# Kernel optimization log

Measured on AMD Instinct MI355X. Metric: run time of the kernel, lower is better.

The kernel has to match this reference:

```python
import jax, jax.numpy as jnp
import numpy as np
from jax import lax


def _conv(x, w, pad):
    # NCHW conv, OIHW weights, stride 1
    return lax.conv_general_dilated(x, w, (1, 1), [(pad, pad), (pad, pad)],
                                    dimension_numbers=('NCHW', 'OIHW', 'NCHW'))


def _cba(x, w, s, b):
    # ConvModule: 3x3 conv (no bias) + folded BN (scale s, bias b) + ReLU
    y = _conv(x, w, 1)
    return jax.nn.relu(y * s[None, :, None, None] + b[None, :, None, None])


def _pam(x, wb, bb, wc, bc, wd, bd, alpha):
    B, C, H, W = x.shape
    fb = (_conv(x, wb, 0) + bb[None, :, None, None]).reshape(B, -1, H * W)  # [B,C/8,HW]
    fc = (_conv(x, wc, 0) + bc[None, :, None, None]).reshape(B, -1, H * W)  # [B,C/8,HW]
    # attention_s = softmax(feat_b^T @ feat_c) over last dim -> [B,HW,HW]
    attn = jax.nn.softmax(jnp.einsum('bcn,bcm->bnm', fb, fc), axis=-1)
    fd = (_conv(x, wd, 0) + bd[None, :, None, None]).reshape(B, C, H * W)
    # feat_d @ attn^T
    fe = jnp.einsum('bcm,bnm->bcn', fd, attn).reshape(B, C, H, W)
    return alpha * fe + x


def _cam(x, beta):
    B, C, H, W = x.shape
    fa = x.reshape(B, C, H * W)
    att = jnp.einsum('bcn,bdn->bcd', fa, fa)  # [B,C,C]
    att = jax.nn.softmax(jnp.max(att, axis=-1, keepdims=True) - att, axis=-1)
    fe = jnp.einsum('bcd,bdn->bcn', att, fa).reshape(B, C, H, W)
    return beta * fe + x


def _up2x(x):
    # bilinear, align_corners=False (half-pixel) == jax.image.resize 'bilinear'
    B, C, H, W = x.shape
    return jax.image.resize(x, (B, C, 2 * H, 2 * W), 'bilinear')


def setup_inputs() -> dict:
    key = jax.random.key(0)
    B, Cin, H, W = 4, 2048, 64, 64
    IC, C8, NC = 512, 64, 81

    def rn(i, shape, scale=0.02):
        return scale * jax.random.normal(jax.random.fold_in(key, i), shape, jnp.float32)

    inp = {
        'x': jax.random.normal(jax.random.fold_in(key, 0), (B, Cin, H, W), jnp.float32),
        'wp1': rn(1, (IC, Cin, 3, 3)), 'sp1': jnp.ones((IC,), jnp.float32), 'bp1': rn(2, (IC,)),
        'wc1': rn(3, (IC, Cin, 3, 3)), 'sc1': jnp.ones((IC,), jnp.float32), 'bc1': rn(4, (IC,)),
        'pam_wb': rn(5, (C8, IC, 1, 1)), 'pam_bb': rn(6, (C8,)),
        'pam_wc': rn(7, (C8, IC, 1, 1)), 'pam_bc': rn(8, (C8,)),
        'pam_wd': rn(9, (IC, IC, 1, 1)), 'pam_bd': rn(10, (IC,)),
        'alpha': rn(11, (1,), 1.0), 'beta': rn(12, (1,), 1.0),
        'wp2': rn(13, (IC, IC, 3, 3)), 'sp2': jnp.ones((IC,), jnp.float32), 'bp2': rn(14, (IC,)),
        'wc2': rn(15, (IC, IC, 3, 3)), 'sc2': jnp.ones((IC,), jnp.float32), 'bc2': rn(16, (IC,)),
        'wlog': rn(17, (NC, IC, 1, 1)), 'blog': rn(18, (NC,)),
        'wp3': rn(19, (NC, IC, 1, 1)), 'bp3': rn(20, (NC,)),
        'wc3': rn(21, (NC, IC, 1, 1)), 'bc3': rn(22, (NC,)),
    }
    return inp


def reference(x, wp1, sp1, bp1, wc1, sc1, bc1,
              pam_wb, pam_bb, pam_wc, pam_bc, pam_wd, pam_bd, alpha, beta,
              wp2, sp2, bp2, wc2, sc2, bc2,
              wlog, blog, wp3, bp3, wc3, bc3):
    feat_p = _cba(x, wp1, sp1, bp1)
    feat_p = _pam(feat_p, pam_wb, pam_bb, pam_wc, pam_bc, pam_wd, pam_bd, alpha)
    feat_p = _cba(feat_p, wp2, sp2, bp2)

    feat_c = _cba(x, wc1, sc1, bc1)
    feat_c = _cam(feat_c, beta)
    feat_c = _cba(feat_c, wc2, sc2, bc2)

    fusion = feat_p + feat_c
    fusion_out = _conv(fusion, wlog, 0) + blog[None, :, None, None]  # dropout = identity (eval)
    p_out = _conv(feat_p, wp3, 0) + bp3[None, :, None, None]
    c_out = _conv(feat_c, wc3, 0) + bc3[None, :, None, None]
    return (_up2x(p_out), _up2x(c_out), _up2x(fusion_out))
```

## Files before the change

kernel.cpp:

```cpp
#include <hip/hip_runtime.h>

typedef unsigned short u16;
typedef __bf16 bf16x8 __attribute__((ext_vector_type(8)));
typedef float f32x4 __attribute__((ext_vector_type(4)));

static __device__ __forceinline__ float bf2f(u16 v){ unsigned u=((unsigned)v)<<16; float f; __builtin_memcpy(&f,&u,4); return f; }
static __device__ __forceinline__ u16 f2bf(float f){ unsigned u; __builtin_memcpy(&u,&f,4); u += 0x7fffu + ((u>>16)&1u); return (u16)(u>>16); }

static __device__ __forceinline__ float wave_max(float v){
#pragma unroll
  for(int o=32;o;o>>=1) v=fmaxf(v,__shfl_xor(v,o,64));
  return v;
}
static __device__ __forceinline__ float wave_sum(float v){
#pragma unroll
  for(int o=32;o;o>>=1) v+=__shfl_xor(v,o,64);
  return v;
}

__global__ void k_sentinel(u16* __restrict__ o, float v){ o[0] = f2bf(v); }

__global__ void k_probe(const unsigned* __restrict__ w, int* __restrict__ flag){
  __shared__ int found;
  if (threadIdx.x==0) found = 0;
  __syncthreads();
  int loc = 0;
  for (int i = threadIdx.x; i < 32768; i += 256){
    unsigned v = w[i];
    if ((((v >> 7) & 0xFFu) == 0xFFu) || (((v >> 23) & 0xFFu) == 0xFFu)) loc = 1;
  }
  if (loc) atomicOr(&found, 1);
  __syncthreads();
  if (threadIdx.x==0) *flag = found;
}

__global__ void k_cvt(const void* __restrict__ src, u16* __restrict__ dst, int n, const int* __restrict__ flag){
  int i = blockIdx.x*256 + threadIdx.x;
  if (i >= n) return;
  if (*flag) dst[i] = f2bf(((const float*)src)[i]);
  else       dst[i] = ((const u16*)src)[i];
}

__global__ void k_zero(uint4* __restrict__ p, long n){
  long i = (long)blockIdx.x*256 + threadIdx.x;
  if (i < n) p[i] = make_uint4(0,0,0,0);
}

__global__ void k_pad1(const void* __restrict__ xb, u16* __restrict__ xp, int ICD, int icoff, int bbase,
                       const int* __restrict__ flag){
  __shared__ u16 tile[64][65];
  const int h = blockIdx.x;
  const int ic0 = blockIdx.y<<6;
  const int bi = blockIdx.z;
  const int t = threadIdx.x, lane = t&63, g = t>>6;
  const size_t base = ((size_t)(bbase+bi)*2048 + icoff + ic0)*4096 + (size_t)h*64;
  if (*flag){
    const float* src = (const float*)xb + base;
#pragma unroll
    for(int i=0;i<16;i++){ int icl = g*16+i; tile[icl][lane] = f2bf(src[(size_t)icl*4096 + lane]); }
  } else {
    const u16* src = (const u16*)xb + base;
#pragma unroll
    for(int i=0;i<16;i++){ int icl = g*16+i; tile[icl][lane] = src[(size_t)icl*4096 + lane]; }
  }
  __syncthreads();
  u16* dst = xp + ((size_t)bi*4356 + ((size_t)(h+1))*66 + 1)*ICD + ic0;
#pragma unroll
  for(int j=0;j<16;j++){ int w = g*16+j; dst[(size_t)w*ICD + lane] = tile[lane][w]; }
}

__global__ void k_wtrans(const void* __restrict__ w, u16* __restrict__ wt, int ICS, int ICD, int icoff,
                         const int* __restrict__ flag){
  size_t i = (size_t)blockIdx.x*256 + threadIdx.x;
  int icd = (int)(i & (ICD-1));
  size_t rest = i / ICD;
  int oc = (int)(rest & 511);
  int tap = (int)(rest >> 9);
  size_t sidx = ((size_t)oc*ICS + icoff + icd)*9 + tap;
  wt[i] = (*flag) ? f2bf(((const float*)w)[sidx]) : ((const u16*)w)[sidx];
}

__global__ void k_transpose(const u16* __restrict__ in, u16* __restrict__ outp, int R, int C){
  __shared__ u16 tile[64][65];
  const int c0 = blockIdx.x<<6, r0 = blockIdx.y<<6;
  const int t=threadIdx.x, lane=t&63, g=t>>6;
#pragma unroll
  for(int i=0;i<16;i++){ int rl=g*16+i; tile[rl][lane] = in[(size_t)(r0+rl)*C + c0 + lane]; }
  __syncthreads();
#pragma unroll
  for(int j=0;j<16;j++){ int cl=g*16+j; outp[(size_t)(c0+cl)*R + r0 + lane] = tile[lane][cl]; }
}

__global__ void k_pad_strip(const u16* __restrict__ in, u16* __restrict__ outp, int C, int npix){
  long i = (long)blockIdx.x*256 + threadIdx.x;
  int vpp = C>>3;
  if (i >= (long)npix*vpp) return;
  int p = (int)(i/vpp), v = (int)(i - (long)p*vpp);
  int b = p>>12, h=(p>>6)&63, w=p&63;
  ((uint4*)outp)[((size_t)(b*66+h+1)*66 + (w+1))*vpp + v] = ((const uint4*)in)[i];
}

__global__ void k_add_bf16(const u16* __restrict__ a, const u16* __restrict__ b, u16* __restrict__ o, long n){
  long i = ((long)blockIdx.x*256 + threadIdx.x)*8;
  if (i >= n) return;
  uint4 va = *(const uint4*)(a+i), vb = *(const uint4*)(b+i);
  u16* pa=(u16*)&va; u16* pb=(u16*)&vb;
  uint4 vo; u16* po=(u16*)&vo;
#pragma unroll
  for(int e=0;e<8;e++) po[e] = f2bf(bf2f(pa[e]) + bf2f(pb[e]));
  *(uint4*)(o+i) = vo;
}

__global__ __launch_bounds__(256,2) void gemm_nt(
    const u16* __restrict__ A, const u16* __restrict__ Bt,
    int N, int K, int lda, int ldb,
    void* __restrict__ Cout, int ldc, int mode,
    const u16* __restrict__ q1, const u16* __restrict__ q2, int zk, long zcb)
{
  if (zk){
    const int zz = blockIdx.z;
    A  += (size_t)zz*zk;
    Bt += (size_t)zz*zk;
    Cout = (void*)((char*)Cout + (size_t)zz*zcb);
    K = zk;
  }
  __shared__ __align__(16) u16 As[128*40];
  __shared__ __align__(16) u16 Bs[128*40];
  const int t = threadIdx.x;
  const int m0 = blockIdx.y<<7, n0 = blockIdx.x<<7;
  const int r = t>>2, q = t&3;
  const u16* A0 = A + (size_t)(m0+r)*lda + q*8;
  const u16* A1 = A0 + (size_t)64*lda;
  const bool bv0 = (n0+r)    < N;
  const bool bv1 = (n0+r+64) < N;
  const u16* B0 = Bt + (size_t)(n0+r)*ldb + q*8;
  const u16* B1 = B0 + (size_t)64*ldb;
  const int wave=t>>6, lane=t&63;
  const int wr=(wave>>1)<<6, wc=(wave&1)<<6, fm=lane&15, kg=lane>>4;
  f32x4 acc[4][4] = {};
  for (int k0=0; k0<K; k0+=32){
    uint4 a0 = *(const uint4*)(A0+k0);
    uint4 a1 = *(const uint4*)(A1+k0);
    uint4 b0 = bv0 ? *(const uint4*)(B0+k0) : make_uint4(0,0,0,0);
    uint4 b1 = bv1 ? *(const uint4*)(B1+k0) : make_uint4(0,0,0,0);
    __syncthreads();
    *(uint4*)&As[r*40+q*8] = a0;
    *(uint4*)&As[(r+64)*40+q*8] = a1;
    *(uint4*)&Bs[r*40+q*8] = b0;
    *(uint4*)&Bs[(r+64)*40+q*8] = b1;
    __syncthreads();
    bf16x8 af[4], bfr[4];
#pragma unroll
    for(int i=0;i<4;i++) af[i]  = *(const bf16x8*)&As[(wr+i*16+fm)*40 + kg*8];
#pragma unroll
    for(int j=0;j<4;j++) bfr[j] = *(const bf16x8*)&Bs[(wc+j*16+fm)*40 + kg*8];
#pragma unroll
    for(int i=0;i<4;i++)
#pragma unroll
      for(int j=0;j<4;j++)
        acc[i][j] = __builtin_amdgcn_mfma_f32_16x16x32_bf16(af[i], bfr[j], acc[i][j], 0,0,0);
  }
  const float alpha = (mode==3) ? bf2f(q1[0]) : 0.f;
#pragma unroll
  for(int j=0;j<4;j++){
    int col = n0 + wc + j*16 + fm;
    if (col >= N) continue;
    float bias = (mode==1) ? bf2f(q1[col]) : 0.f;
#pragma unroll
    for(int i=0;i<4;i++){
      int row = m0 + wr + i*16 + (kg<<2);
#pragma unroll
      for(int rr=0;rr<4;rr++){
        long idx = (long)(row+rr)*ldc + col;
        float v = acc[i][j][rr];
        if (mode==4)      ((float*)Cout)[idx] = v;
        else if (mode==3) ((u16*)Cout)[idx] = f2bf(alpha*v + bf2f(q2[idx]));
        else if (mode==5) ((u16*)Cout)[idx] = f2bf(v + bf2f(q1[row+rr]));
        else if (mode==1) ((u16*)Cout)[idx] = f2bf(v + bias);
        else              ((u16*)Cout)[idx] = f2bf(v);
      }
    }
  }
}

__global__ __launch_bounds__(256,2) void conv3_gemm(
    const u16* __restrict__ Xp, const u16* __restrict__ Wt, int ICt,
    u16* __restrict__ Out, const u16* __restrict__ scale, const u16* __restrict__ bias, int phase,
    long wstr, long ostr)
{
  __shared__ __align__(16) u16 As[128*40];
  __shared__ __align__(16) u16 Bs[128*40];
  const int t = threadIdx.x;
  const int bx = blockIdx.x;
  const int brn = bx>>2;
  const int m0 = blockIdx.y<<7, n0 = (bx&3)<<7;
  const u16* Wb = Wt + (size_t)brn*wstr;
  u16* Ob = Out + (size_t)brn*ostr;
  const u16* scb = scale + brn*1024;
  const u16* bib = bias + brn*1024;
  const int r = t>>2, q = t&3;
  const int p0 = m0 + r, p1 = p0 + 64;
  const size_t xb0 = ((size_t)((p0>>12)*66 + ((p0>>6)&63))*66 + (p0&63))*ICt + q*8;
  const size_t xb1 = ((size_t)((p1>>12)*66 + ((p1>>6)&63))*66 + (p1&63))*ICt + q*8;
  const u16* W0 = Wb + (size_t)(n0+r)*ICt + q*8;
  const u16* W1 = W0 + (size_t)64*ICt;
  const size_t wtap = (size_t)512*ICt;
  const int wave=t>>6, lane=t&63;
  const int wr=(wave>>1)<<6, wc=(wave&1)<<6, fm=lane&15, kg=lane>>4;
  f32x4 acc[4][4] = {};
  for (int tap=0; tap<9; tap++){
    const size_t toff = (size_t)((tap/3)*66 + (tap%3))*ICt;
    const u16* xa0 = Xp + xb0 + toff;
    const u16* xa1 = Xp + xb1 + toff;
    const u16* wa0 = W0 + (size_t)tap*wtap;
    const u16* wa1 = W1 + (size_t)tap*wtap;
    for (int k0=0; k0<ICt; k0+=32){
      uint4 a0 = *(const uint4*)(xa0+k0);
      uint4 a1 = *(const uint4*)(xa1+k0);
      uint4 b0 = *(const uint4*)(wa0+k0);
      uint4 b1 = *(const uint4*)(wa1+k0);
      __syncthreads();
      *(uint4*)&As[r*40+q*8] = a0;
      *(uint4*)&As[(r+64)*40+q*8] = a1;
      *(uint4*)&Bs[r*40+q*8] = b0;
      *(uint4*)&Bs[(r+64)*40+q*8] = b1;
      __syncthreads();
      bf16x8 af[4], bfr[4];
#pragma unroll
      for(int i=0;i<4;i++) af[i]  = *(const bf16x8*)&As[(wr+i*16+fm)*40 + kg*8];
#pragma unroll
      for(int j=0;j<4;j++) bfr[j] = *(const bf16x8*)&Bs[(wc+j*16+fm)*40 + kg*8];
#pragma unroll
      for(int i=0;i<4;i++)
#pragma unroll
        for(int j=0;j<4;j++)
          acc[i][j] = __builtin_amdgcn_mfma_f32_16x16x32_bf16(af[i], bfr[j], acc[i][j], 0,0,0);
    }
  }
#pragma unroll
  for(int j=0;j<4;j++){
    int col = n0 + wc + j*16 + fm;
    float s = bf2f(scb[col]), bb = bf2f(bib[col]);
#pragma unroll
    for(int i=0;i<4;i++){
      int row = m0 + wr + i*16 + (kg<<2);
#pragma unroll
      for(int rr=0;rr<4;rr++){
        size_t idx = (size_t)(row+rr)*512 + col;
        float v = acc[i][j][rr];
        if (phase == 0)      Ob[idx] = f2bf(v);
        else if (phase == 1) Ob[idx] = f2bf(fmaxf(s*(bf2f(Ob[idx]) + v) + bb, 0.f));
        else                 Ob[idx] = f2bf(fmaxf(s*v + bb, 0.f));
      }
    }
  }
}

__global__ __launch_bounds__(256) void k_softmax_pam(u16* __restrict__ attn){
  __shared__ float red[8];
  u16* row = attn + (size_t)blockIdx.x*4096;
  uint4* rv = (uint4*)row;
  const int t = threadIdx.x;
  uint4 c0 = rv[2*t], c1 = rv[2*t+1];
  u16* e0 = (u16*)&c0; u16* e1=(u16*)&c1;
  float v[16];
#pragma unroll
  for(int i=0;i<8;i++){ v[i]=bf2f(e0[i]); v[8+i]=bf2f(e1[i]); }
  float mx = v[0];
#pragma unroll
  for(int i=1;i<16;i++) mx = fmaxf(mx, v[i]);
  mx = wave_max(mx);
  if((t&63)==0) red[t>>6] = mx;
  __syncthreads();
  mx = fmaxf(fmaxf(red[0],red[1]),fmaxf(red[2],red[3]));
  float s = 0.f;
#pragma unroll
  for(int i=0;i<16;i++){ v[i]=__expf(v[i]-mx); s += v[i]; }
  s = wave_sum(s);
  if((t&63)==0) red[4+(t>>6)] = s;
  __syncthreads();
  s = red[4]+red[5]+red[6]+red[7];
  float inv = 1.f/s;
#pragma unroll
  for(int i=0;i<8;i++){ e0[i]=f2bf(v[i]*inv); e1[i]=f2bf(v[8+i]*inv); }
  rv[2*t]=c0; rv[2*t+1]=c1;
}

__global__ __launch_bounds__(256) void k_pv_combine(const float* __restrict__ Pp, u16* __restrict__ io,
                                                    const u16* __restrict__ alpha){
  const int i = blockIdx.x*256 + threadIdx.x;
  const float4* p = (const float4*)Pp;
  float4 a0 = p[i], a1 = p[i+262144], a2 = p[i+524288], a3 = p[i+786432];
  const float al = bf2f(alpha[0]);
  ushort4 d = ((const ushort4*)io)[i];
  ushort4 o;
  o.x = f2bf(al*(a0.x+a1.x+a2.x+a3.x) + bf2f(d.x));
  o.y = f2bf(al*(a0.y+a1.y+a2.y+a3.y) + bf2f(d.y));
  o.z = f2bf(al*(a0.z+a1.z+a2.z+a3.z) + bf2f(d.z));
  o.w = f2bf(al*(a0.w+a1.w+a2.w+a3.w) + bf2f(d.w));
  ((ushort4*)io)[i] = o;
}

__global__ __launch_bounds__(256) void k_softmax_cam8(const float* __restrict__ P8, u16* __restrict__ outp){
  __shared__ float red[8];
  const int t = threadIdx.x;
  const float* r0 = P8 + (size_t)blockIdx.x*512;
  float a = 0.f, b2 = 0.f;
#pragma unroll
  for(int s2=0;s2<8;s2++){ a += r0[(size_t)s2*262144 + t]; b2 += r0[(size_t)s2*262144 + 256 + t]; }
  a = -a; b2 = -b2;
  float mx = wave_max(fmaxf(a,b2));
  if((t&63)==0) red[t>>6]=mx;
  __syncthreads();
  mx = fmaxf(fmaxf(red[0],red[1]),fmaxf(red[2],red[3]));
  float ea = __expf(a-mx), eb = __expf(b2-mx);
  float s = wave_sum(ea+eb);
  if((t&63)==0) red[4+(t>>6)]=s;
  __syncthreads();
  s = red[4]+red[5]+red[6]+red[7];
  float inv = 1.f/s;
  u16* orow = outp + (size_t)blockIdx.x*512;
  orow[t] = f2bf(ea*inv); orow[t+256] = f2bf(eb*inv);
}

__global__ __launch_bounds__(128) void k_upsample(const u16* __restrict__ hp, const u16* __restrict__ hc,
                                                  const u16* __restrict__ hf, void* __restrict__ outp,
                                                  const int* __restrict__ flag){
  int bx = blockIdx.x;
  const int y = bx & 127; bx >>= 7;
  const int ch = bx % 81; bx /= 81;
  const int b = bx & 3; const int head = bx >> 2;
  const u16* src = (head==0) ? hp : (head==1 ? hc : hf);
  const int xo = threadIdx.x;
  float fy = y*0.5f - 0.25f, fx = xo*0.5f - 0.25f;
  float fy0 = floorf(fy), fx0 = floorf(fx);
  float wy = fy - fy0, wx = fx - fx0;
  int y0 = max((int)fy0, 0), y1 = min((int)fy0 + 1, 63);
  int x0 = max((int)fx0, 0), x1 = min((int)fx0 + 1, 63);
  const size_t bb = (size_t)b*4096;
  float v00 = bf2f(src[(bb + y0*64 + x0)*81 + ch]);
  float v01 = bf2f(src[(bb + y0*64 + x1)*81 + ch]);
  float v10 = bf2f(src[(bb + y1*64 + x0)*81 + ch]);
  float v11 = bf2f(src[(bb + y1*64 + x1)*81 + ch]);
  float v = (1.f-wy)*((1.f-wx)*v00 + wx*v01) + wy*((1.f-wx)*v10 + wx*v11);
  size_t oidx = ((size_t)(head*324 + b*81 + ch))*16384 + (size_t)y*128 + xo;
  if (*flag) ((float*)outp)[oidx] = v;
  else       ((u16*)outp)[oidx]  = f2bf(v);
}

extern "C" void kernel_launch(void* const* d_in, const int* in_sizes, int n_in,
                              void* d_out, int out_size, void* d_ws, size_t ws_size,
                              hipStream_t stream)
{
  (void)in_sizes; (void)n_in;
  const void* x   = d_in[0];
  const void* wp1 = d_in[1];
  const void* wc1 = d_in[4];
  const void* wp2 = d_in[15];
  const void* wc2 = d_in[18];
  char* ws = (char*)d_ws;
  const size_t MB = 1048576;
  auto P = [&](size_t off){ return (u16*)(ws + off); };

  if (ws_size < 58*MB || (long)out_size*2 < (long)18*MB){
    k_sentinel<<<1,1,0,stream>>>((u16*)d_out, 16.0f * (float)(ws_size / MB));
    return;
  }

  const size_t FP1=0, FC1=16*MB, WTCP=32*MB, WTCC=41*MB,
               FB=32*MB, FCc=34*MB, FDTb=36*MB, PP=40*MB,
               FATb=32*MB, FEATC=40*MB,
               WT2P=16*MB, WT2C=WT2P+4718592,
               FUS=16*MB, HP=32*MB, HC=35*MB, HF=38*MB;
  u16* prm = P(56*MB);
  int* FLAG = (int*)(ws + 57*MB + 524288);
  u16* SCR = (u16*)d_out;
  const int SP1=0, BP1=512, SC1=1024, BC1=1536, SP2=2048, BP2=2560, SC2=3072, BC2=3584,
            PBB=4096, PBC=4160, PBD=4224, BP3=4736, BC3=4817, BLOG=4898, ALPHA=4979, BETA=4980,
            PWB=4992, PWC=37760, PWD=70528, W3P=332672, W3C=374144, W3L=415616;

  k_probe<<<1, 256, 0, stream>>>((const unsigned*)x, FLAG);
  auto cv = [&](int di, int po, int n){
    k_cvt<<<(n+255)/256, 256, 0, stream>>>(d_in[di], prm+po, n, FLAG);
  };
  cv(2,SP1,512);  cv(3,BP1,512);  cv(5,SC1,512);  cv(6,BC1,512);
  cv(16,SP2,512); cv(17,BP2,512); cv(19,SC2,512); cv(20,BC2,512);
  cv(8,PBB,64);   cv(10,PBC,64);  cv(12,PBD,512);
  cv(24,BP3,81);  cv(26,BC3,81);  cv(22,BLOG,81);
  cv(13,ALPHA,1); cv(14,BETA,1);
  cv(7,PWB,32768); cv(9,PWC,32768); cv(11,PWD,262144);
  cv(23,W3P,41472); cv(25,W3C,41472); cv(21,W3L,41472);

  const int BPD = 2;
  const int nbp = 4/BPD;
  k_zero<<<BPD*2178, 256, 0, stream>>>((uint4*)SCR, (long)BPD*557568);
  for (int ch=0; ch<2; ch++){
    k_wtrans<<<18432, 256, 0, stream>>>(wp1, P(WTCP), 2048, 1024, ch*1024, FLAG);
    k_wtrans<<<18432, 256, 0, stream>>>(wc1, P(WTCC), 2048, 1024, ch*1024, FLAG);
    for (int bp=0; bp<nbp; bp++){
      k_pad1<<<dim3(64,16,BPD), 256, 0, stream>>>(x, SCR, 1024, ch*1024, bp*BPD, FLAG);
      const size_t ob = (size_t)bp*BPD*4096*512;
      conv3_gemm<<<dim3(8,32*BPD), 256, 0, stream>>>(SCR, P(WTCP), 1024, P(FP1)+ob, prm+SP1, prm+BP1, ch,
                                                     4718592L, 8388608L);
    }
  }

  gemm_nt<<<dim3(1,128), 256, 0, stream>>>(P(FP1), prm+PWB, 64, 512, 512, 512, P(FB), 64, 1, prm+PBB, nullptr, 0, 0);
  gemm_nt<<<dim3(1,128), 256, 0, stream>>>(P(FP1), prm+PWC, 64, 512, 512, 512, P(FCc), 64, 1, prm+PBC, nullptr, 0, 0);
  for (int b=0;b<4;b++){
    const size_t fo = (size_t)b*4096*64, so = (size_t)b*4096*512;
    gemm_nt<<<dim3(32,4), 256, 0, stream>>>(prm+PWD, P(FP1)+so, 4096, 512, 512, 512, P(FDTb), 4096, 5, prm+PBD, nullptr, 0, 0);
    for (int ck=0;ck<2;ck++){
      gemm_nt<<<dim3(32,16), 256, 0, stream>>>(P(FB)+fo+(size_t)ck*131072, P(FCc)+fo, 4096, 64, 64, 64, SCR, 4096, 0, nullptr, nullptr, 0, 0);
      k_softmax_pam<<<2048, 256, 0, stream>>>(SCR);
      gemm_nt<<<dim3(4,16,4), 256, 0, stream>>>(SCR, P(FDTb), 512, 4096, 4096, 4096, (void*)P(PP), 512, 4, nullptr, nullptr, 1024, 4194304);
      k_pv_combine<<<1024, 256, 0, stream>>>((const float*)P(PP), P(FP1)+so+(size_t)ck*1048576, prm+ALPHA);
    }
  }

  u16* ATTCS = SCR + 4194304;
  for (int b=0;b<4;b++){
    const size_t so = (size_t)b*4096*512;
    k_transpose<<<dim3(8,64), 256, 0, stream>>>(P(FC1)+so, P(FATb), 4096, 512);
    gemm_nt<<<dim3(4,4,8), 256, 0, stream>>>(P(FATb), P(FATb), 512, 4096, 4096, 4096, (void*)SCR, 512, 4, nullptr, nullptr, 512, 1048576);
    k_softmax_cam8<<<512, 256, 0, stream>>>((const float*)SCR, ATTCS);
    gemm_nt<<<dim3(4,32), 256, 0, stream>>>(P(FC1)+so, ATTCS, 512, 512, 512, 512, P(FEATC)+so, 512, 3, prm+BETA, P(FC1)+so, 0, 0);
  }

  k_wtrans<<<9216, 256, 0, stream>>>(wp2, P(WT2P), 512, 512, 0, FLAG);
  k_wtrans<<<9216, 256, 0, stream>>>(wc2, P(WT2C), 512, 512, 0, FLAG);
  k_zero<<<4356, 256, 0, stream>>>((uint4*)SCR, 1115136);
  k_pad_strip<<<4096, 256, 0, stream>>>(P(FP1), SCR, 512, 16384);
  conv3_gemm<<<dim3(4,128), 256, 0, stream>>>(SCR, P(WT2P), 512, P(FP1), prm+SP2, prm+BP2, 2, 0L, 0L);
  k_pad_strip<<<4096, 256, 0, stream>>>(P(FEATC), SCR, 512, 16384);
  conv3_gemm<<<dim3(4,128), 256, 0, stream>>>(SCR, P(WT2C), 512, P(FEATC), prm+SC2, prm+BC2, 2, 0L, 0L);

  k_add_bf16<<<4096, 256, 0, stream>>>(P(FP1), P(FEATC), P(FUS), (long)16384*512);
  gemm_nt<<<dim3(1,128), 256, 0, stream>>>(P(FP1), prm+W3P, 81, 512, 512, 512, P(HP), 81, 1, prm+BP3, nullptr, 0, 0);
  gemm_nt<<<dim3(1,128), 256, 0, stream>>>(P(FEATC), prm+W3C, 81, 512, 512, 512, P(HC), 81, 1, prm+BC3, nullptr, 0, 0);
  gemm_nt<<<dim3(1,128), 256, 0, stream>>>(P(FUS), prm+W3L, 81, 512, 512, 512, P(HF), 81, 1, prm+BLOG, nullptr, 0, 0);
  k_upsample<<<124416, 128, 0, stream>>>(P(HP), P(HC), P(HF), d_out, FLAG);
}
```

Measured before the change: 2.474 ms.

## Rework weight transpose, conv tile order, tap/k loop order, and fuse PAM projections

Replaces the per-element weight transpose with a kernel that reads nine contiguous taps per thread and writes coalesced along input channels. In conv3_gemm, the block index is swizzled so consecutive blocks spread across eight M groups, and the tap and K loops are swapped so each K slice covers all nine taps in turn. The two PAM 1x1 projections (b and c) become a single GEMM with 128 outputs, and the attention GEMM reads both halves from that buffer with stride 128. Together these aim to cut uncoalesced weight reads, improve L2 reuse in the conv, and remove one launch, but the swizzle assumes gridDim.y is a multiple of 8.

```diff
diff --git a/kernel.cpp b/kernel.cpp
--- a/kernel.cpp
+++ b/kernel.cpp
@@ -69,15 +69,24 @@
   for(int j=0;j<16;j++){ int w = g*16+j; dst[(size_t)w*ICD + lane] = tile[lane][w]; }
 }
 
-__global__ void k_wtrans(const void* __restrict__ w, u16* __restrict__ wt, int ICS, int ICD, int icoff,
-                         const int* __restrict__ flag){
-  size_t i = (size_t)blockIdx.x*256 + threadIdx.x;
-  int icd = (int)(i & (ICD-1));
-  size_t rest = i / ICD;
-  int oc = (int)(rest & 511);
-  int tap = (int)(rest >> 9);
-  size_t sidx = ((size_t)oc*ICS + icoff + icd)*9 + tap;
-  wt[i] = (*flag) ? f2bf(((const float*)w)[sidx]) : ((const u16*)w)[sidx];
+__global__ void k_wtrans2(const void* __restrict__ w, u16* __restrict__ wt, int ICS, int ICD, int icoff,
+                          const int* __restrict__ flag){
+  const int l = threadIdx.x & 63, g = threadIdx.x >> 6;
+  const int icd = (blockIdx.x<<6) + l;
+  const int oc  = (blockIdx.y<<2) + g;
+  const size_t sbase = ((size_t)oc*ICS + icoff + icd)*9;
+  float v[9];
+  if (*flag){
+    const float* s = (const float*)w + sbase;
+#pragma unroll
+    for(int t=0;t<9;t++) v[t] = s[t];
+  } else {
+    const u16* s = (const u16*)w + sbase;
+#pragma unroll
+    for(int t=0;t<9;t++) v[t] = bf2f(s[t]);
+  }
+#pragma unroll
+  for(int t=0;t<9;t++) wt[((size_t)t*512 + oc)*ICD + icd] = f2bf(v[t]);
 }
 
 __global__ void k_transpose(const u16* __restrict__ in, u16* __restrict__ outp, int R, int C){
@@ -191,9 +200,13 @@
   __shared__ __align__(16) u16 As[128*40];
   __shared__ __align__(16) u16 Bs[128*40];
   const int t = threadIdx.x;
-  const int bx = blockIdx.x;
-  const int brn = bx>>2;
-  const int m0 = blockIdx.y<<7, n0 = (bx&3)<<7;
+  const int per8 = gridDim.y >> 3;
+  const int lid = blockIdx.x + blockIdx.y*gridDim.x;
+  const int k8 = lid & 7, jj = lid >> 3;
+  const int mt = k8*per8 + (jj & (per8-1));
+  const int nbr = jj / per8;
+  const int brn = nbr>>2;
+  const int m0 = mt<<7, n0 = (nbr&3)<<7;
   const u16* Wb = Wt + (size_t)brn*wstr;
   u16* Ob = Out + (size_t)brn*ostr;
   const u16* scb = scale + brn*1024;
@@ -208,17 +221,17 @@
   const int wave=t>>6, lane=t&63;
   const int wr=(wave>>1)<<6, wc=(wave&1)<<6, fm=lane&15, kg=lane>>4;
   f32x4 acc[4][4] = {};
-  for (int tap=0; tap<9; tap++){
-    const size_t toff = (size_t)((tap/3)*66 + (tap%3))*ICt;
-    const u16* xa0 = Xp + xb0 + toff;
-    const u16* xa1 = Xp + xb1 + toff;
-    const u16* wa0 = W0 + (size_t)tap*wtap;
-    const u16* wa1 = W1 + (size_t)tap*wtap;
-    for (int k0=0; k0<ICt; k0+=32){
-      uint4 a0 = *(const uint4*)(xa0+k0);
-      uint4 a1 = *(const uint4*)(xa1+k0);
-      uint4 b0 = *(const uint4*)(wa0+k0);
-      uint4 b1 = *(const uint4*)(wa1+k0);
+  for (int k0=0; k0<ICt; k0+=32){
+    for (int tap=0; tap<9; tap++){
+      const size_t toff = (size_t)((tap/3)*66 + (tap%3))*ICt + k0;
+      const u16* xa0 = Xp + xb0 + toff;
+      const u16* xa1 = Xp + xb1 + toff;
+      const u16* wa0 = W0 + (size_t)tap*wtap + k0;
+      const u16* wa1 = W1 + (size_t)tap*wtap + k0;
+      uint4 a0 = *(const uint4*)(xa0);
+      uint4 a1 = *(const uint4*)(xa1);
+      uint4 b0 = *(const uint4*)(wa0);
+      uint4 b1 = *(const uint4*)(wa1);
       __syncthreads();
       *(uint4*)&As[r*40+q*8] = a0;
       *(uint4*)&As[(r+64)*40+q*8] = a1;
@@ -368,7 +381,7 @@
   }
 
   const size_t FP1=0, FC1=16*MB, WTCP=32*MB, WTCC=41*MB,
-               FB=32*MB, FCc=34*MB, FDTb=36*MB, PP=40*MB,
+               FB=32*MB, FDTb=36*MB, PP=40*MB,
                FATb=32*MB, FEATC=40*MB,
                WT2P=16*MB, WT2C=WT2P+4718592,
                FUS=16*MB, HP=32*MB, HC=35*MB, HF=38*MB;
@@ -395,8 +408,8 @@
   const int nbp = 4/BPD;
   k_zero<<<BPD*2178, 256, 0, stream>>>((uint4*)SCR, (long)BPD*557568);
   for (int ch=0; ch<2; ch++){
-    k_wtrans<<<18432, 256, 0, stream>>>(wp1, P(WTCP), 2048, 1024, ch*1024, FLAG);
-    k_wtrans<<<18432, 256, 0, stream>>>(wc1, P(WTCC), 2048, 1024, ch*1024, FLAG);
+    k_wtrans2<<<dim3(16,128), 256, 0, stream>>>(wp1, P(WTCP), 2048, 1024, ch*1024, FLAG);
+    k_wtrans2<<<dim3(16,128), 256, 0, stream>>>(wc1, P(WTCC), 2048, 1024, ch*1024, FLAG);
     for (int bp=0; bp<nbp; bp++){
       k_pad1<<<dim3(64,16,BPD), 256, 0, stream>>>(x, SCR, 1024, ch*1024, bp*BPD, FLAG);
       const size_t ob = (size_t)bp*BPD*4096*512;
@@ -405,13 +418,12 @@
     }
   }
 
-  gemm_nt<<<dim3(1,128), 256, 0, stream>>>(P(FP1), prm+PWB, 64, 512, 512, 512, P(FB), 64, 1, prm+PBB, nullptr, 0, 0);
-  gemm_nt<<<dim3(1,128), 256, 0, stream>>>(P(FP1), prm+PWC, 64, 512, 512, 512, P(FCc), 64, 1, prm+PBC, nullptr, 0, 0);
+  gemm_nt<<<dim3(1,128), 256, 0, stream>>>(P(FP1), prm+PWB, 128, 512, 512, 512, P(FB), 128, 1, prm+PBB, nullptr, 0, 0);
   for (int b=0;b<4;b++){
-    const size_t fo = (size_t)b*4096*64, so = (size_t)b*4096*512;
+    const size_t fo = (size_t)b*4096*128, so = (size_t)b*4096*512;
     gemm_nt<<<dim3(32,4), 256, 0, stream>>>(prm+PWD, P(FP1)+so, 4096, 512, 512, 512, P(FDTb), 4096, 5, prm+PBD, nullptr, 0, 0);
     for (int ck=0;ck<2;ck++){
-      gemm_nt<<<dim3(32,16), 256, 0, stream>>>(P(FB)+fo+(size_t)ck*131072, P(FCc)+fo, 4096, 64, 64, 64, SCR, 4096, 0, nullptr, nullptr, 0, 0);
+      gemm_nt<<<dim3(32,16), 256, 0, stream>>>(P(FB)+fo+(size_t)ck*262144, P(FB)+64+fo, 4096, 64, 128, 128, SCR, 4096, 0, nullptr, nullptr, 0, 0);
       k_softmax_pam<<<2048, 256, 0, stream>>>(SCR);
       gemm_nt<<<dim3(4,16,4), 256, 0, stream>>>(SCR, P(FDTb), 512, 4096, 4096, 4096, (void*)P(PP), 512, 4, nullptr, nullptr, 1024, 4194304);
       k_pv_combine<<<1024, 256, 0, stream>>>((const float*)P(PP), P(FP1)+so+(size_t)ck*1048576, prm+ALPHA);
@@ -427,8 +439,8 @@
     gemm_nt<<<dim3(4,32), 256, 0, stream>>>(P(FC1)+so, ATTCS, 512, 512, 512, 512, P(FEATC)+so, 512, 3, prm+BETA, P(FC1)+so, 0, 0);
   }
 
-  k_wtrans<<<9216, 256, 0, stream>>>(wp2, P(WT2P), 512, 512, 0, FLAG);
-  k_wtrans<<<9216, 256, 0, stream>>>(wc2, P(WT2C), 512, 512, 0, FLAG);
+  k_wtrans2<<<dim3(8,128), 256, 0, stream>>>(wp2, P(WT2P), 512, 512, 0, FLAG);
+  k_wtrans2<<<dim3(8,128), 256, 0, stream>>>(wc2, P(WT2C), 512, 512, 0, FLAG);
   k_zero<<<4356, 256, 0, stream>>>((uint4*)SCR, 1115136);
   k_pad_strip<<<4096, 256, 0, stream>>>(P(FP1), SCR, 512, 16384);
   conv3_gemm<<<dim3(4,128), 256, 0, stream>>>(SCR, P(WT2P), 512, P(FP1), prm+SP2, prm+BP2, 2, 0L, 0L);
```

Measured after the change: 2.414 ms. 1.02x faster.
